# Kernel tuning notes

Measured on AMD Instinct MI355X. Metric: run time of the kernel, lower is better.

The kernel has to match this reference:

```python
import jax, jax.numpy as jnp
import numpy as np

NEG_BIG = -1e9

def setup_inputs() -> dict:
    key = jax.random.key(0)
    kq, kk, kv, kwq, kwk, kwv, km = jax.random.split(key, 7)
    B, S, d = 16, 1024, 512
    Q = jax.random.normal(kq, (B, S, d), dtype=jnp.float32)
    K = jax.random.normal(kk, (B, S, d), dtype=jnp.float32)
    V = jax.random.normal(kv, (B, S, d), dtype=jnp.float32)
    # nn.Linear weights [d, d]; torch applies x @ W.T
    WQ = jax.random.normal(kwq, (d, d), dtype=jnp.float32) / np.sqrt(d)
    WK = jax.random.normal(kwk, (d, d), dtype=jnp.float32) / np.sqrt(d)
    WV = jax.random.normal(kwv, (d, d), dtype=jnp.float32) / np.sqrt(d)
    mask = jax.random.randint(km, (B, S), 0, 2, dtype=jnp.int32)
    return {"Q": Q, "K": K, "V": V, "WQ": WQ, "WK": WK, "WV": WV, "mask": mask}


def reference(Q, K, V, WQ, WK, WV, mask):
    d = Q.shape[-1]
    q = jnp.einsum('bsd,ed->bse', Q, WQ)
    k = jnp.einsum('bsd,ed->bse', K, WK)
    v = jnp.einsum('bsd,ed->bse', V, WV)
    scores = jnp.einsum('bqd,bkd->bqk', q, k) / jnp.sqrt(jnp.float32(d))
    attn = jax.nn.softmax(scores, axis=-1)
    # Faithful to original: mask applied AFTER softmax with -1e9 fill
    m = mask[:, None, :]  # [B,1,S] broadcast over query dim
    attn = jnp.where(m == 0, jnp.float32(NEG_BIG), attn)
    out = jnp.einsum('bqk,bkd->bqd', attn, v)
    return (out, attn)
```

## Files before the change

### kernel.cpp

```cpp
#include <hip/hip_runtime.h>
#include <hip/hip_bf16.h>

typedef float f32x4 __attribute__((ext_vector_type(4)));
typedef __bf16 bf16x8 __attribute__((ext_vector_type(8)));
typedef unsigned short u16x8 __attribute__((ext_vector_type(8)));
typedef unsigned short u16x4 __attribute__((ext_vector_type(4)));
typedef int i32x4 __attribute__((ext_vector_type(4)));

#define NEG_BIG_F (-1000000000.0f)
#define SCALE_F 0.044194173824159216f

__device__ __forceinline__ unsigned short f2bf(float f) {
  unsigned int u = __float_as_uint(f);
  u += 0x7FFFu + ((u >> 16) & 1u);
  return (unsigned short)(u >> 16);
}

__device__ __forceinline__ float bf2f(unsigned short h) {
  return __uint_as_float((unsigned int)h << 16);
}

__device__ __forceinline__ u16x8 cvt8(f32x4 a, f32x4 b) {
  u16x8 r;
  r[0] = f2bf(a[0]); r[1] = f2bf(a[1]); r[2] = f2bf(a[2]); r[3] = f2bf(a[3]);
  r[4] = f2bf(b[0]); r[5] = f2bf(b[1]); r[6] = f2bf(b[2]); r[7] = f2bf(b[3]);
  return r;
}

__device__ __forceinline__ bf16x8 u2b(u16x8 u) {
  union { u16x8 u; bf16x8 b; } c; c.u = u; return c.b;
}

__device__ __forceinline__ void gload16(const void* g, char* l) {
  __builtin_amdgcn_global_load_lds(
      (const __attribute__((address_space(1))) unsigned int*)g,
      (__attribute__((address_space(3))) unsigned int*)l, 16, 0, 0);
}

__global__ __launch_bounds__(256) void cvtWX(
    const float* __restrict__ w0, const float* __restrict__ w1,
    const float* __restrict__ w2, const float* __restrict__ Q,
    const float* __restrict__ Kx,
    unsigned short* __restrict__ wb, unsigned short* __restrict__ xb)
{
  const int z = blockIdx.z;
  if (z == 0) {
    if (blockIdx.x >= 384) return;
    const int i = (blockIdx.x * 256 + threadIdx.x) * 8;
    const float* src = i < 262144 ? w0 : (i < 524288 ? w1 : w2);
    const int j = i & 262143;
    f32x4 a = *(const f32x4*)(src + j);
    f32x4 b = *(const f32x4*)(src + j + 4);
    *(u16x8*)&wb[i] = cvt8(a, b);
  } else {
    const float* src = z == 1 ? Q : Kx;
    unsigned short* dst = xb + (size_t)(z - 1) * 8388608;
    const int i = (blockIdx.x * 256 + threadIdx.x) * 8;
    f32x4 a = *(const f32x4*)(src + i);
    f32x4 b = *(const f32x4*)(src + i + 4);
    *(u16x8*)&dst[i] = cvt8(a, b);
  }
}

__global__ __launch_bounds__(512, 2) void proj_all(
    const unsigned short* __restrict__ xb, const float* __restrict__ V,
    const unsigned short* __restrict__ wb,
    unsigned short* __restrict__ qb, unsigned short* __restrict__ kb,
    unsigned short* __restrict__ vt)
{
  __shared__ __align__(16) char pool[81920];

  const int bid = blockIdx.x;
  const int tid = threadIdx.x;
  const int lane = tid & 63, wave = tid >> 6;
  const int fr = lane & 15, fq = lane >> 4;

  if (bid < 256) {
    unsigned short (*As)[256][32] = (unsigned short (*)[256][32])pool;
    unsigned short (*Bs)[256][32] = (unsigned short (*)[256][32])(pool + 32768);

    const int z = bid >> 7, rem = bid & 127;
    const int m0 = (rem & 63) * 256, n0 = (rem >> 6) * 256;
    const unsigned short* Abase = xb + (size_t)z * 8388608 + (size_t)m0 * 512;
    const unsigned short* Bbase = wb + (size_t)z * 262144 + (size_t)n0 * 512;
    const int wr = (wave >> 2) * 128, wc = (wave & 3) * 64;

    f32x4 acc[8][4] = {};

    const unsigned short* gA[2]; char* lA[2];
    const unsigned short* gB[2]; char* lB[2];
    #pragma unroll
    for (int i = 0; i < 2; i++) {
      const int c = tid + 512 * i, row = c >> 2, slot = c & 3;
      const int sw = (slot ^ ((row >> 1) & 3)) * 8;
      gA[i] = Abase + (size_t)row * 512 + sw;
      gB[i] = Bbase + (size_t)row * 512 + sw;
      lA[i] = pool + c * 16;
      lB[i] = pool + 32768 + c * 16;
    }

    #pragma unroll
    for (int i = 0; i < 2; i++) { gload16(gA[i], lA[i]); gload16(gB[i], lB[i]); }

    int cur = 0;
    for (int kt = 0; kt < 512; kt += 32) {
      const int nb = cur ^ 1;
      if (kt < 480) {
        #pragma unroll
        for (int i = 0; i < 2; i++) {
          gload16(gA[i] + kt + 32, lA[i] + nb * 16384);
          gload16(gB[i] + kt + 32, lB[i] + nb * 16384);
        }
        asm volatile("s_waitcnt vmcnt(4) lgkmcnt(0)" ::: "memory");
      } else {
        asm volatile("s_waitcnt vmcnt(0) lgkmcnt(0)" ::: "memory");
      }
      __builtin_amdgcn_sched_barrier(0);
      __builtin_amdgcn_s_barrier();

      bf16x8 bv[4];
      #pragma unroll
      for (int nf = 0; nf < 4; nf++) {
        const int br = wc + nf * 16 + fr;
        bv[nf] = *(const bf16x8*)&Bs[cur][br][(fq ^ ((br >> 1) & 3)) * 8];
      }
      #pragma unroll
      for (int mf = 0; mf < 8; mf++) {
        const int ar = wr + mf * 16 + fr;
        bf16x8 av = *(const bf16x8*)&As[cur][ar][(fq ^ ((ar >> 1) & 3)) * 8];
        #pragma unroll
        for (int nf = 0; nf < 4; nf++)
          acc[mf][nf] = __builtin_amdgcn_mfma_f32_16x16x32_bf16(av, bv[nf], acc[mf][nf], 0, 0, 0);
      }
      __builtin_amdgcn_s_barrier();
      cur = nb;
    }

    unsigned short* Y = z ? kb : qb;
    #pragma unroll
    for (int mf = 0; mf < 8; mf++)
      #pragma unroll
      for (int nf = 0; nf < 4; nf++)
        #pragma unroll
        for (int rr = 0; rr < 4; rr++) {
          const int m = m0 + wr + mf * 16 + fq * 4 + rr;
          const int n = n0 + wc + nf * 16 + fr;
          Y[(size_t)m * 512 + n] = f2bf(acc[mf][nf][rr]);
        }
  } else {
    unsigned short (*As)[128][32] = (unsigned short (*)[128][32])pool;
    float          (*Bf)[256][32] = (float (*)[256][32])(pool + 16384);

    const int bid2 = bid - 256;
    const int m0 = (bid2 & 3) * 128, n0 = ((bid2 >> 2) & 3) * 256, b = bid2 >> 4;
    const int wr = (wave >> 2) * 64, wc = (wave & 3) * 64;
    const unsigned short* wv = wb + 524288;

    f32x4 acc[4][4] = {};

    const int arw = tid >> 2, asl = tid & 3;
    const unsigned short* gA = wv + (size_t)(m0 + arw) * 512 + (asl ^ ((arw >> 1) & 3)) * 8;
    char* lA = pool + tid * 16;
    const float* gB[4]; char* lB[4];
    #pragma unroll
    for (int i = 0; i < 4; i++) {
      const int c = tid + 512 * i, row = c >> 3, slot = c & 7;
      gB[i] = V + ((size_t)b * 1024 + n0 + row) * 512 + (slot ^ (row & 7)) * 4;
      lB[i] = pool + 16384 + c * 16;
    }

    gload16(gA, lA);
    #pragma unroll
    for (int i = 0; i < 4; i++) gload16(gB[i], lB[i]);

    int cur = 0;
    for (int kt = 0; kt < 512; kt += 32) {
      const int nb = cur ^ 1;
      if (kt < 480) {
        gload16(gA + kt + 32, lA + nb * 8192);
        #pragma unroll
        for (int i = 0; i < 4; i++) gload16(gB[i] + kt + 32, lB[i] + nb * 32768);
        asm volatile("s_waitcnt vmcnt(5) lgkmcnt(0)" ::: "memory");
      } else {
        asm volatile("s_waitcnt vmcnt(0) lgkmcnt(0)" ::: "memory");
      }
      __builtin_amdgcn_sched_barrier(0);
      __builtin_amdgcn_s_barrier();

      bf16x8 av[4], bv[4];
      #pragma unroll
      for (int mf = 0; mf < 4; mf++) {
        const int ar = wr + mf * 16 + fr;
        av[mf] = *(const bf16x8*)&As[cur][ar][(fq ^ ((ar >> 1) & 3)) * 8];
      }
      #pragma unroll
      for (int nf = 0; nf < 4; nf++) {
        const int br = wc + nf * 16 + fr;
        f32x4 lo = *(const f32x4*)&Bf[cur][br][((fq * 2)     ^ (br & 7)) * 4];
        f32x4 hi = *(const f32x4*)&Bf[cur][br][((fq * 2 + 1) ^ (br & 7)) * 4];
        bv[nf] = u2b(cvt8(lo, hi));
      }
      #pragma unroll
      for (int mf = 0; mf < 4; mf++)
        #pragma unroll
        for (int nf = 0; nf < 4; nf++)
          acc[mf][nf] = __builtin_amdgcn_mfma_f32_16x16x32_bf16(av[mf], bv[nf], acc[mf][nf], 0, 0, 0);
      __builtin_amdgcn_s_barrier();
      cur = nb;
    }

    #pragma unroll
    for (int mf = 0; mf < 4; mf++)
      #pragma unroll
      for (int nf = 0; nf < 4; nf++)
        #pragma unroll
        for (int rr = 0; rr < 4; rr++) {
          const int e = m0 + wr + mf * 16 + fq * 4 + rr;
          const int s = n0 + wc + nf * 16 + fr;
          vt[((size_t)b * 512 + e) * 1024 + s] = f2bf(acc[mf][nf][rr]);
        }
  }
}

__global__ __launch_bounds__(512, 2) void score_mv(
    const unsigned short* __restrict__ qb, const unsigned short* __restrict__ kb,
    const unsigned short* __restrict__ vt, const int* __restrict__ mask,
    unsigned short* __restrict__ P, float* __restrict__ partial,
    float* __restrict__ mvsum)
{
  __shared__ __align__(16) unsigned short As[2][256][32];
  __shared__ __align__(16) unsigned short Bs[2][128][32];

  const int bid = blockIdx.x;
  const int tid = threadIdx.x;

  if (bid >= 512) {
    const int row = (bid - 512) * 8 + (tid >> 6);
    const int b = row >> 9;
    const int lane = tid & 63;
    const unsigned short* vr = vt + (size_t)row * 1024 + lane * 16;
    const int* mr = mask + b * 1024 + lane * 16;
    u16x8 v0 = *(const u16x8*)(vr);
    u16x8 v1 = *(const u16x8*)(vr + 8);
    float s = 0.f;
    #pragma unroll
    for (int j = 0; j < 8; j++) {
      if (!mr[j])     s += bf2f(v0[j]);
      if (!mr[8 + j]) s += bf2f(v1[j]);
    }
    #pragma unroll
    for (int o = 32; o > 0; o >>= 1) s += __shfl_xor(s, o);
    if (lane == 0) mvsum[row] = s;
    return;
  }

  const int xcd = bid & 7, idx = bid >> 3;
  const int bz = xcd * 2 + (idx >> 5);
  const int tile = idx & 31;
  const int m0 = (tile & 3) * 256;
  const int ntile = tile >> 2;
  const int n0 = ntile * 128;
  const int lane = tid & 63, wave = tid >> 6;
  const int wr = (wave >> 1) * 64, wc = (wave & 1) * 64;
  const int fr = lane & 15, fq = lane >> 4;

  f32x4 acc[4][4] = {};

  const unsigned short* gA[2]; char* lA[2];
  #pragma unroll
  for (int i = 0; i < 2; i++) {
    const int c = tid + 512 * i, row = c >> 2, slot = c & 3;
    gA[i] = qb + ((size_t)bz * 1024 + m0 + row) * 512 + (slot ^ ((row >> 1) & 3)) * 8;
    lA[i] = (char*)&As[0][0][0] + c * 16;
  }
  const int brw = tid >> 2, bsl = tid & 3;
  const unsigned short* gB = kb + ((size_t)bz * 1024 + n0 + brw) * 512 + (bsl ^ ((brw >> 1) & 3)) * 8;
  char* lB = (char*)&Bs[0][0][0] + tid * 16;

  #pragma unroll
  for (int i = 0; i < 2; i++) gload16(gA[i], lA[i]);
  gload16(gB, lB);

  int cur = 0;
  for (int kt = 0; kt < 512; kt += 32) {
    const int nb = cur ^ 1;
    if (kt < 480) {
      #pragma unroll
      for (int i = 0; i < 2; i++) gload16(gA[i] + kt + 32, lA[i] + nb * 16384);
      gload16(gB + kt + 32, lB + nb * 8192);
      asm volatile("s_waitcnt vmcnt(3) lgkmcnt(0)" ::: "memory");
    } else {
      asm volatile("s_waitcnt vmcnt(0) lgkmcnt(0)" ::: "memory");
    }
    __builtin_amdgcn_sched_barrier(0);
    __builtin_amdgcn_s_barrier();

    bf16x8 bv[4];
    #pragma unroll
    for (int nf = 0; nf < 4; nf++) {
      const int br = wc + nf * 16 + fr;
      bv[nf] = *(const bf16x8*)&Bs[cur][br][(fq ^ ((br >> 1) & 3)) * 8];
    }
    #pragma unroll
    for (int mf = 0; mf < 4; mf++) {
      const int ar = wr + mf * 16 + fr;
      bf16x8 av = *(const bf16x8*)&As[cur][ar][(fq ^ ((ar >> 1) & 3)) * 8];
      #pragma unroll
      for (int nf = 0; nf < 4; nf++)
        acc[mf][nf] = __builtin_amdgcn_mfma_f32_16x16x32_bf16(av, bv[nf], acc[mf][nf], 0, 0, 0);
    }
    __builtin_amdgcn_s_barrier();
    cur = nb;
  }

  int mcol[4];
  #pragma unroll
  for (int nf = 0; nf < 4; nf++)
    mcol[nf] = mask[bz * 1024 + n0 + wc + nf * 16 + fr];

  unsigned short* Pb = P + ((size_t)bz << 20);
  const int slot = ntile * 2 + (wave & 1);
  #pragma unroll
  for (int mf = 0; mf < 4; mf++) {
    #pragma unroll
    for (int rr = 0; rr < 4; rr++) {
      const int m = m0 + wr + mf * 16 + fq * 4 + rr;
      float e = 0.f;
      #pragma unroll
      for (int nf = 0; nf < 4; nf++) {
        const float ev = __expf(acc[mf][nf][rr] * SCALE_F);
        e += ev;
        Pb[(size_t)m * 1024 + n0 + wc + nf * 16 + fr] =
            mcol[nf] ? f2bf(ev) : (unsigned short)0;
      }
      e += __shfl_xor(e, 1); e += __shfl_xor(e, 2);
      e += __shfl_xor(e, 4); e += __shfl_xor(e, 8);
      if (fr == 0)
        partial[(size_t)slot * 16384 + bz * 1024 + m] = e;
    }
  }
}

__global__ __launch_bounds__(512) void pv_attn(
    const unsigned short* __restrict__ P, const unsigned short* __restrict__ vt,
    const float* __restrict__ partial, const float* __restrict__ mvsum,
    const int* __restrict__ mask,
    float* __restrict__ out, float* __restrict__ attn)
{
  __shared__ __align__(16) unsigned short As[2][64][32];
  __shared__ __align__(16) unsigned short Bs[2][512][32];
  __shared__ float inv_l[64];

  const int tid = threadIdx.x;
  const int lin = blockIdx.x;
  const int xcd = lin & 7, idx = lin >> 3;
  const int bz = xcd * 2 + (idx >> 4);
  const int m0 = (idx & 15) * 64;
  const int lane = tid & 63, wave = tid >> 6;
  const int n0 = wave * 64;
  const int fr = lane & 15, fq = lane >> 4;

  f32x4 acc[4][4] = {};

  if (tid < 64) {
    float s = 0.f;
    #pragma unroll
    for (int p = 0; p < 16; p++) s += partial[(size_t)p * 16384 + bz * 1024 + m0 + tid];
    inv_l[tid] = 1.0f / s;
  }

  const unsigned short* gA = nullptr; char* lA = nullptr;
  if (tid < 256) {
    const int row = tid >> 2, slot = tid & 3;
    gA = P + ((size_t)bz << 20) + (size_t)(m0 + row) * 1024 + (slot ^ ((row >> 1) & 3)) * 8;
    lA = (char*)&As[0][0][0] + tid * 16;
  }
  const unsigned short* gB[4]; char* lB[4];
  #pragma unroll
  for (int i = 0; i < 4; i++) {
    const int c = tid + 512 * i, row = c >> 2, slot = c & 3;
    gB[i] = vt + ((size_t)bz * 512 + row) * 1024 + (slot ^ ((row >> 1) & 3)) * 8;
    lB[i] = (char*)&Bs[0][0][0] + c * 16;
  }

  const int arow = tid >> 3, acol = (tid & 7) * 4;
  const int aslot8 = ((acol >> 3) ^ ((arow >> 1) & 3)) * 8 + (acol & 7);
  float* arp = attn + ((size_t)bz * 1024 + m0 + arow) * 1024 + acol;
  const int* mrp = mask + bz * 1024 + acol;

  if (tid < 256) gload16(gA, lA);
  #pragma unroll
  for (int i = 0; i < 4; i++) gload16(gB[i], lB[i]);
  __syncthreads();

  int cur = 0;
  for (int t = 0; t < 32; t++) {
    const int nb = cur ^ 1;
    const int kt = t * 32;
    if (t < 31) {
      if (tid < 256) gload16(gA + kt + 32, lA + nb * 4096);
      #pragma unroll
      for (int i = 0; i < 4; i++) gload16(gB[i] + kt + 32, lB[i] + nb * 32768);
      if (wave < 4) asm volatile("s_waitcnt vmcnt(5) lgkmcnt(0)" ::: "memory");
      else          asm volatile("s_waitcnt vmcnt(4) lgkmcnt(0)" ::: "memory");
    } else {
      asm volatile("s_waitcnt vmcnt(0) lgkmcnt(0)" ::: "memory");
    }
    __builtin_amdgcn_sched_barrier(0);
    __builtin_amdgcn_s_barrier();

    bf16x8 af[4], bv[4];
    #pragma unroll
    for (int mf = 0; mf < 4; mf++) {
      const int ar = mf * 16 + fr;
      af[mf] = *(const bf16x8*)&As[cur][ar][(fq ^ ((ar >> 1) & 3)) * 8];
    }
    #pragma unroll
    for (int nf = 0; nf < 4; nf++) {
      const int br = n0 + nf * 16 + fr;
      bv[nf] = *(const bf16x8*)&Bs[cur][br][(fq ^ ((br >> 1) & 3)) * 8];
    }
    #pragma unroll
    for (int mf = 0; mf < 4; mf++)
      #pragma unroll
      for (int nf = 0; nf < 4; nf++)
        acc[mf][nf] = __builtin_amdgcn_mfma_f32_16x16x32_bf16(af[mf], bv[nf], acc[mf][nf], 0, 0, 0);

    {
      const u16x4 pv4 = *(const u16x4*)&As[cur][arow][aslot8];
      const i32x4 mv = *(const i32x4*)(mrp + kt);
      const float iv = inv_l[arow];
      f32x4 o;
      o[0] = mv[0] ? bf2f(pv4[0]) * iv : NEG_BIG_F;
      o[1] = mv[1] ? bf2f(pv4[1]) * iv : NEG_BIG_F;
      o[2] = mv[2] ? bf2f(pv4[2]) * iv : NEG_BIG_F;
      o[3] = mv[3] ? bf2f(pv4[3]) * iv : NEG_BIG_F;
      *(f32x4*)(arp + kt) = o;
    }
    __builtin_amdgcn_s_barrier();
    cur = nb;
  }

  float mvv[4];
  #pragma unroll
  for (int nf = 0; nf < 4; nf++)
    mvv[nf] = mvsum[bz * 512 + n0 + nf * 16 + fr];
  #pragma unroll
  for (int mf = 0; mf < 4; mf++)
    #pragma unroll
    for (int rr = 0; rr < 4; rr++) {
      const int m = m0 + mf * 16 + fq * 4 + rr;
      const float iv = inv_l[mf * 16 + fq * 4 + rr];
      #pragma unroll
      for (int nf = 0; nf < 4; nf++)
        out[((size_t)bz * 1024 + m) * 512 + n0 + nf * 16 + fr] =
            iv * acc[mf][nf][rr] + NEG_BIG_F * mvv[nf];
    }
}

extern "C" void kernel_launch(void* const* d_in, const int* in_sizes, int n_in,
                              void* d_out, int out_size, void* d_ws, size_t ws_size,
                              hipStream_t stream)
{
  const float* Q  = (const float*)d_in[0];
  const float* Kx = (const float*)d_in[1];
  const float* V  = (const float*)d_in[2];
  const float* WQ = (const float*)d_in[3];
  const float* WK = (const float*)d_in[4];
  const float* WV = (const float*)d_in[5];
  const int* mask = (const int*)d_in[6];

  const int B = 16, S = 1024, D = 512;
  float* out_f  = (float*)d_out;
  float* attn_f = out_f + (size_t)B * S * D;
  unsigned short* Pbuf = (unsigned short*)d_out;
  unsigned short* xb = (unsigned short*)attn_f;

  unsigned short* qb = (unsigned short*)d_ws;
  unsigned short* kb = qb + (size_t)B * S * D;
  unsigned short* vt = kb + (size_t)B * S * D;
  unsigned short* wb = vt + (size_t)B * S * D;
  float* partial = (float*)(wb + 786432);
  float* mvsum = partial + 262144;

  cvtWX<<<dim3(4096, 1, 3), 256, 0, stream>>>(WQ, WK, WV, Q, Kx, wb, xb);
  proj_all<<<dim3(512), 512, 0, stream>>>(xb, V, wb, qb, kb, vt);
  score_mv<<<dim3(1536), 512, 0, stream>>>(qb, kb, vt, mask, Pbuf, partial, mvsum);
  pv_attn<<<dim3(256), 512, 0, stream>>>(Pbuf, vt, partial, mvsum, mask, out_f, attn_f);
}
```

Before: 137.1 us.

## Fold WQ and WK into one combined matrix, skipping the K projection

Scores q·k^T equal Q·(WQ^T WK)·K^T, so the change precomputes M = WQ^T·WK (a 512x512 fp32 product done with scalar FMAs inside the convert kernel) and projects only Q through M. Raw K is converted to bf16 and used directly as the key operand, which removes the K-projection GEMM and cuts the projection grid from 512 to 384 blocks. The cost is a naive 512^3 scalar matmul in the convert kernel with strided WQ reads. It also adds a bf16 rounding of M and of raw K, which may shift numerical error.

Result: slower. 161.6 us (+17.8%).

```diff
diff --git a/kernel.cpp b/kernel.cpp
--- a/kernel.cpp
+++ b/kernel.cpp
@@ -38,24 +38,43 @@
 }
 
 __global__ __launch_bounds__(256) void cvtWX(
-    const float* __restrict__ w0, const float* __restrict__ w1,
-    const float* __restrict__ w2, const float* __restrict__ Q,
+    const float* __restrict__ WQ, const float* __restrict__ WK,
+    const float* __restrict__ WV, const float* __restrict__ Q,
     const float* __restrict__ Kx,
-    unsigned short* __restrict__ wb, unsigned short* __restrict__ xb)
+    unsigned short* __restrict__ wb, unsigned short* __restrict__ xb,
+    unsigned short* __restrict__ kb)
 {
   const int z = blockIdx.z;
+  const int bid = blockIdx.x;
   if (z == 0) {
-    if (blockIdx.x >= 384) return;
-    const int i = (blockIdx.x * 256 + threadIdx.x) * 8;
-    const float* src = i < 262144 ? w0 : (i < 524288 ? w1 : w2);
-    const int j = i & 262143;
-    f32x4 a = *(const f32x4*)(src + j);
-    f32x4 b = *(const f32x4*)(src + j + 4);
-    *(u16x8*)&wb[i] = cvt8(a, b);
+    if (bid < 128) {
+      const int i = (bid * 256 + threadIdx.x) * 8;
+      f32x4 a = *(const f32x4*)(WV + i);
+      f32x4 b = *(const f32x4*)(WV + i + 4);
+      *(u16x8*)&wb[i] = cvt8(a, b);
+    } else if (bid < 384) {
+      const int g = (bid - 128) * 256 + threadIdx.x;
+      const int i = g & 511, j0 = (g >> 9) * 4;
+      float a0 = 0.f, a1 = 0.f, a2 = 0.f, a3 = 0.f;
+      #pragma unroll 4
+      for (int e = 0; e < 512; e++) {
+        const float qv = WQ[e * 512 + i];
+        const float* wkr = WK + e * 512 + j0;
+        a0 += qv * wkr[0];
+        a1 += qv * wkr[1];
+        a2 += qv * wkr[2];
+        a3 += qv * wkr[3];
+      }
+      unsigned short* mt = wb + 262144;
+      mt[(j0 + 0) * 512 + i] = f2bf(a0);
+      mt[(j0 + 1) * 512 + i] = f2bf(a1);
+      mt[(j0 + 2) * 512 + i] = f2bf(a2);
+      mt[(j0 + 3) * 512 + i] = f2bf(a3);
+    }
   } else {
     const float* src = z == 1 ? Q : Kx;
-    unsigned short* dst = xb + (size_t)(z - 1) * 8388608;
-    const int i = (blockIdx.x * 256 + threadIdx.x) * 8;
+    unsigned short* dst = z == 1 ? xb : kb;
+    const int i = (bid * 256 + threadIdx.x) * 8;
     f32x4 a = *(const f32x4*)(src + i);
     f32x4 b = *(const f32x4*)(src + i + 4);
     *(u16x8*)&dst[i] = cvt8(a, b);
@@ -65,8 +84,7 @@
 __global__ __launch_bounds__(512, 2) void proj_all(
     const unsigned short* __restrict__ xb, const float* __restrict__ V,
     const unsigned short* __restrict__ wb,
-    unsigned short* __restrict__ qb, unsigned short* __restrict__ kb,
-    unsigned short* __restrict__ vt)
+    unsigned short* __restrict__ qb, unsigned short* __restrict__ vt)
 {
   __shared__ __align__(16) char pool[81920];
 
@@ -75,14 +93,13 @@
   const int lane = tid & 63, wave = tid >> 6;
   const int fr = lane & 15, fq = lane >> 4;
 
-  if (bid < 256) {
+  if (bid < 128) {
     unsigned short (*As)[256][32] = (unsigned short (*)[256][32])pool;
     unsigned short (*Bs)[256][32] = (unsigned short (*)[256][32])(pool + 32768);
 
-    const int z = bid >> 7, rem = bid & 127;
-    const int m0 = (rem & 63) * 256, n0 = (rem >> 6) * 256;
-    const unsigned short* Abase = xb + (size_t)z * 8388608 + (size_t)m0 * 512;
-    const unsigned short* Bbase = wb + (size_t)z * 262144 + (size_t)n0 * 512;
+    const int m0 = (bid & 63) * 256, n0 = (bid >> 6) * 256;
+    const unsigned short* Abase = xb + (size_t)m0 * 512;
+    const unsigned short* Bbase = wb + 262144 + (size_t)n0 * 512;
     const int wr = (wave >> 2) * 128, wc = (wave & 3) * 64;
 
     f32x4 acc[8][4] = {};
@@ -136,7 +153,6 @@
       cur = nb;
     }
 
-    unsigned short* Y = z ? kb : qb;
     #pragma unroll
     for (int mf = 0; mf < 8; mf++)
       #pragma unroll
@@ -145,16 +161,16 @@
         for (int rr = 0; rr < 4; rr++) {
           const int m = m0 + wr + mf * 16 + fq * 4 + rr;
           const int n = n0 + wc + nf * 16 + fr;
-          Y[(size_t)m * 512 + n] = f2bf(acc[mf][nf][rr]);
+          qb[(size_t)m * 512 + n] = f2bf(acc[mf][nf][rr]);
         }
   } else {
     unsigned short (*As)[128][32] = (unsigned short (*)[128][32])pool;
     float          (*Bf)[256][32] = (float (*)[256][32])(pool + 16384);
 
-    const int bid2 = bid - 256;
+    const int bid2 = bid - 128;
     const int m0 = (bid2 & 3) * 128, n0 = ((bid2 >> 2) & 3) * 256, b = bid2 >> 4;
     const int wr = (wave >> 2) * 64, wc = (wave & 3) * 64;
-    const unsigned short* wv = wb + 524288;
+    const unsigned short* wv = wb;
 
     f32x4 acc[4][4] = {};
 
@@ -483,8 +499,8 @@
   float* partial = (float*)(wb + 786432);
   float* mvsum = partial + 262144;
 
-  cvtWX<<<dim3(4096, 1, 3), 256, 0, stream>>>(WQ, WK, WV, Q, Kx, wb, xb);
-  proj_all<<<dim3(512), 512, 0, stream>>>(xb, V, wb, qb, kb, vt);
+  cvtWX<<<dim3(4096, 1, 3), 256, 0, stream>>>(WQ, WK, WV, Q, Kx, wb, xb, kb);
+  proj_all<<<dim3(384), 512, 0, stream>>>(xb, V, wb, qb, vt);
   score_mv<<<dim3(1536), 512, 0, stream>>>(qb, kb, vt, mask, Pbuf, partial, mvsum);
   pv_attn<<<dim3(256), 512, 0, stream>>>(Pbuf, vt, partial, mvsum, mask, out_f, attn_f);
 }
```
